# Performance work log

Measured on AMD Instinct MI355X. Metric: run time of the kernel, lower is better.

## Reference

```python
import jax, jax.numpy as jnp
import numpy as np

N = 100_000
E = 1_600_000
F_IN = 128
HID = 128
OUT = 64


def setup_inputs() -> dict:
    key = jax.random.key(0)
    k = jax.random.split(key, 6)
    x = jax.random.normal(k[0], (N, F_IN), dtype=jnp.float32)
    edge_index = jax.random.randint(k[1], (2, E), 0, N, dtype=jnp.int64)
    edge_weight = jax.random.uniform(k[2], (E,), dtype=jnp.float32)
    W1 = jax.random.normal(k[3], (F_IN, HID), dtype=jnp.float32) * (1.0 / np.sqrt(F_IN))
    b1 = jnp.zeros((HID,), dtype=jnp.float32)
    W2 = jax.random.normal(k[4], (HID, OUT), dtype=jnp.float32) * (1.0 / np.sqrt(HID))
    b2 = jnp.zeros((OUT,), dtype=jnp.float32)
    return {"x": x, "edge_index": edge_index, "edge_weight": edge_weight,
            "W1": W1, "b1": b1, "W2": W2, "b2": b2}


def reference(x, edge_index, edge_weight, W1, b1, W2, b2):
    n = x.shape[0]
    src, dst = edge_index[0], edge_index[1]
    # gcn_norm: add self-loops with weight 1
    loop = jnp.arange(n, dtype=src.dtype)
    src_f = jnp.concatenate([src, loop])          # [E+N]
    dst_f = jnp.concatenate([dst, loop])          # [E+N]
    w_f = jnp.concatenate([edge_weight, jnp.ones((n,), dtype=edge_weight.dtype)])
    # degree over target nodes, symmetric normalization D^-1/2 A D^-1/2
    deg = jax.ops.segment_sum(w_f, dst_f, num_segments=n)   # [N]
    dinv = jnp.where(deg > 0, jax.lax.rsqrt(deg), 0.0)
    norm = dinv[src_f] * w_f * dinv[dst_f]        # [E+N]
    # GCNConv: linear transform then normalized sparse aggregation + bias
    h = x @ W1                                    # [N, HID]
    msg = h[src_f] * norm[:, None]                # [E+N, HID] gather
    agg = jax.ops.segment_sum(msg, dst_f, num_segments=n) + b1  # scatter-add
    # ReLU + Linear
    return jax.nn.relu(agg) @ W2 + b2             # [N, OUT]
```

## Files before the change

### kernel.cpp

```cpp
#include <hip/hip_runtime.h>

#define N_NODES 100000
#define N_EDGES 1600000
#define F_IN    128
#define HID     128
#define F_OUT   64

#define NBUCK   196
#define NCHB    256
#define CHUNK_E (N_EDGES / NCHB)
#define GHN     (NBUCK * NCHB)

#define XB_BLKS (N_NODES * 16 / 256)
#define WC_BLKS ((HID * F_IN + F_OUT * HID + 255) / 256)

typedef __attribute__((ext_vector_type(8))) short bf16x8;
typedef __attribute__((ext_vector_type(4))) float f32x4;


__device__ __forceinline__ unsigned int bf16rn(float f) {
    unsigned int u = __float_as_uint(f);
    return (u + 0x7fffu + ((u >> 16) & 1u)) >> 16;
}
__device__ __forceinline__ float bf16tof(unsigned short h) {
    return __uint_as_float(((unsigned int)h) << 16);
}


__global__ __launch_bounds__(256) void k_pre(
        const float* __restrict__ x, unsigned short* __restrict__ xh,
        const float* __restrict__ W1, const float* __restrict__ W2,
        unsigned short* __restrict__ w1t, unsigned short* __restrict__ w2t,
        const int* __restrict__ dst, int* __restrict__ ghist) {
    __shared__ int bins[NBUCK];
    const int blk = blockIdx.x;
    const int t = threadIdx.x;
    if (blk < XB_BLKS) {
        int i = blk * 256 + t;
        float4 a = ((const float4*)x)[2 * i];
        float4 b = ((const float4*)x)[2 * i + 1];
        uint4 r;
        r.x = bf16rn(a.x) | (bf16rn(a.y) << 16);
        r.y = bf16rn(a.z) | (bf16rn(a.w) << 16);
        r.z = bf16rn(b.x) | (bf16rn(b.y) << 16);
        r.w = bf16rn(b.z) | (bf16rn(b.w) << 16);
        ((uint4*)xh)[i] = r;
    } else if (blk < XB_BLKS + WC_BLKS) {
        int i = (blk - XB_BLKS) * 256 + t;
        if (i < HID * F_IN) {
            int n = i >> 7, k = i & 127;
            w1t[i] = (unsigned short)bf16rn(W1[k * HID + n]);
        }
        int j = i - HID * F_IN;
        if (j >= 0 && j < F_OUT * HID) {
            int n = j >> 7, k = j & 127;
            w2t[j] = (unsigned short)bf16rn(W2[k * F_OUT + n]);
        }
    } else {
        int cb = blk - XB_BLKS - WC_BLKS;
        for (int j = t; j < NBUCK; j += 256) bins[j] = 0;
        __syncthreads();
        const int base = cb * CHUNK_E;
        for (int i = t; i < CHUNK_E; i += 256)
            atomicAdd(&bins[dst[base + i] >> 9], 1);
        __syncthreads();
        for (int j = t; j < NBUCK; j += 256)
            ghist[j * NCHB + cb] = bins[j];
    }
}


__global__ void k_scan_part(const int* __restrict__ data, int* __restrict__ part, int n) {
    int i = blockIdx.x * 256 + threadIdx.x;
    int v = (i < n) ? data[i] : 0;
    #pragma unroll
    for (int off = 32; off > 0; off >>= 1) v += __shfl_down(v, off, 64);
    __shared__ int ws[4];
    if ((threadIdx.x & 63) == 0) ws[threadIdx.x >> 6] = v;
    __syncthreads();
    if (threadIdx.x == 0) part[blockIdx.x] = ws[0] + ws[1] + ws[2] + ws[3];
}

__global__ __launch_bounds__(512) void k_scan_top(int* __restrict__ part, int nparts) {
    __shared__ int s[512];
    int t = threadIdx.x;
    int v = (t < nparts) ? part[t] : 0;
    s[t] = v;
    __syncthreads();
    for (int off = 1; off < 512; off <<= 1) {
        int u = (t >= off) ? s[t - off] : 0;
        __syncthreads();
        s[t] += u;
        __syncthreads();
    }
    if (t < nparts) part[t] = s[t] - v;
}

__global__ void k_scan_down(int* __restrict__ data, const int* __restrict__ part, int n) {
    __shared__ int s[256];
    int t = threadIdx.x;
    int i = blockIdx.x * 256 + t;
    int v = (i < n) ? data[i] : 0;
    s[t] = v;
    __syncthreads();
    for (int off = 1; off < 256; off <<= 1) {
        int u = (t >= off) ? s[t - off] : 0;
        __syncthreads();
        s[t] += u;
        __syncthreads();
    }
    if (i < n) data[i] = part[blockIdx.x] + s[t] - v;
}


__global__ __launch_bounds__(256) void k_bscatter(const int* __restrict__ src,
                                                  const int* __restrict__ dst,
                                                  const float* __restrict__ w,
                                                  const int* __restrict__ ghist,
                                                  int2* __restrict__ spw) {
    __shared__ int cur[NBUCK];
    const int t = threadIdx.x;
    const int blk = blockIdx.x;
    for (int j = t; j < NBUCK; j += 256) cur[j] = ghist[j * NCHB + blk];
    __syncthreads();
    const int base = blk * CHUNK_E;
    for (int i = t; i < CHUNK_E; i += 256) {
        int e = base + i;
        int d = dst[e];
        int b = d >> 9;
        int pos = atomicAdd(&cur[b], 1);
        int2 p;
        p.x = src[e] | ((d & 511) << 17);
        p.y = __float_as_int(w[e]);
        spw[pos] = p;
    }
}


__global__ __launch_bounds__(512) void k_csr(const int2* __restrict__ spw,
                                             const int* __restrict__ ghist,
                                             int* __restrict__ row_ptr,
                                             float* __restrict__ dinv,
                                             int2* __restrict__ pairs) {
    __shared__ int   scnt[512];
    __shared__ float swsum[512];
    __shared__ int   sexcl[512];
    const int t = threadIdx.x;
    const int b = blockIdx.x;
    const int bstart = ghist[b * NCHB];
    const int bend   = (b == NBUCK - 1) ? N_EDGES : ghist[(b + 1) * NCHB];
    const int ne = bend - bstart;

    scnt[t] = 0; swsum[t] = 0.0f;
    __syncthreads();
    for (int i = t; i < ne; i += 512) {
        int2 pe = spw[bstart + i];
        int dl = pe.x >> 17;
        atomicAdd(&scnt[dl], 1);
        atomicAdd(&swsum[dl], __int_as_float(pe.y));
    }
    __syncthreads();

    sexcl[t] = scnt[t];
    __syncthreads();
    for (int off = 1; off < 512; off <<= 1) {
        int u = (t >= off) ? sexcl[t - off] : 0;
        __syncthreads();
        sexcl[t] += u;
        __syncthreads();
    }
    int excl = sexcl[t] - scnt[t];

    int node = b * 512 + t;
    if (node < N_NODES) {
        row_ptr[node] = bstart + excl;
        dinv[node] = rsqrtf(1.0f + swsum[t]);
    }
    if (b == NBUCK - 1 && t == 0) row_ptr[N_NODES] = N_EDGES;

    sexcl[t] = excl;
    __syncthreads();
    scnt[t] = 0;
    __syncthreads();

    for (int i = t; i < ne; i += 512) {
        int2 pe = spw[bstart + i];
        int dl = pe.x >> 17;
        int r = atomicAdd(&scnt[dl], 1);
        int2 q;
        q.x = pe.x & 0x1FFFF;
        q.y = pe.y;
        pairs[bstart + sexcl[dl] + r] = q;
    }
}


__global__ __launch_bounds__(512) void k_gmlp(
        const int2* __restrict__ pairs,
        const int* __restrict__ row_ptr,
        const float* __restrict__ dinv,
        const unsigned short* __restrict__ xh,
        const unsigned short* __restrict__ w1t,
        const float* __restrict__ b1,
        const unsigned short* __restrict__ w2t,
        const float* __restrict__ b2,
        float* __restrict__ out) {
    __shared__ unsigned short gt[16][128];
    __shared__ unsigned short ht[16][128];

    const int t = threadIdx.x;
    const int row0 = blockIdx.x * 16;

    {
        const int grp  = t >> 5;
        const int lane = t & 31;
        const int n = row0 + grp;
        const float dn = dinv[n];
        const ushort4* xh4 = (const ushort4*)xh;

        ushort4 sv = xh4[n * 32 + lane];
        float4 acc;
        acc.x = dn * bf16tof(sv.x);
        acc.y = dn * bf16tof(sv.y);
        acc.z = dn * bf16tof(sv.z);
        acc.w = dn * bf16tof(sv.w);

        int beg = row_ptr[n];
        int end = row_ptr[n + 1];
        int e = beg;
        for (; e + 3 < end; e += 4) {
            int2 p0 = pairs[e];
            int2 p1 = pairs[e + 1];
            int2 p2 = pairs[e + 2];
            int2 p3 = pairs[e + 3];
            float nw0 = dinv[p0.x] * __int_as_float(p0.y);
            float nw1 = dinv[p1.x] * __int_as_float(p1.y);
            float nw2 = dinv[p2.x] * __int_as_float(p2.y);
            float nw3 = dinv[p3.x] * __int_as_float(p3.y);
            ushort4 v0 = xh4[p0.x * 32 + lane];
            ushort4 v1 = xh4[p1.x * 32 + lane];
            ushort4 v2 = xh4[p2.x * 32 + lane];
            ushort4 v3 = xh4[p3.x * 32 + lane];
            acc.x += nw0 * bf16tof(v0.x); acc.y += nw0 * bf16tof(v0.y);
            acc.z += nw0 * bf16tof(v0.z); acc.w += nw0 * bf16tof(v0.w);
            acc.x += nw1 * bf16tof(v1.x); acc.y += nw1 * bf16tof(v1.y);
            acc.z += nw1 * bf16tof(v1.z); acc.w += nw1 * bf16tof(v1.w);
            acc.x += nw2 * bf16tof(v2.x); acc.y += nw2 * bf16tof(v2.y);
            acc.z += nw2 * bf16tof(v2.z); acc.w += nw2 * bf16tof(v2.w);
            acc.x += nw3 * bf16tof(v3.x); acc.y += nw3 * bf16tof(v3.y);
            acc.z += nw3 * bf16tof(v3.z); acc.w += nw3 * bf16tof(v3.w);
        }
        for (; e < end; ++e) {
            int2 p = pairs[e];
            float nw = dinv[p.x] * __int_as_float(p.y);
            ushort4 v = xh4[p.x * 32 + lane];
            acc.x += nw * bf16tof(v.x); acc.y += nw * bf16tof(v.y);
            acc.z += nw * bf16tof(v.z); acc.w += nw * bf16tof(v.w);
        }
        acc.x *= dn; acc.y *= dn; acc.z *= dn; acc.w *= dn;

        uint2 r;
        r.x = bf16rn(acc.x) | (bf16rn(acc.y) << 16);
        r.y = bf16rn(acc.z) | (bf16rn(acc.w) << 16);
        *(uint2*)&gt[grp][(lane * 4) ^ ((grp & 7) << 3)] = r;
    }
    __syncthreads();

    const int wv   = t >> 6;
    const int lane = t & 63;
    const int r16  = lane & 15;
    const int g    = lane >> 4;
    const int swr  = (r16 & 7) << 3;

    {
        bf16x8 a[4];
        #pragma unroll
        for (int kt = 0; kt < 4; ++kt)
            a[kt] = *(const bf16x8*)&gt[r16][(kt * 32 + g * 8) ^ swr];

        f32x4 acc = {0.f, 0.f, 0.f, 0.f};
        const unsigned short* bcol = w1t + (wv * 16 + r16) * HID + g * 8;
        #pragma unroll
        for (int kt = 0; kt < 4; ++kt) {
            bf16x8 b = *(const bf16x8*)(bcol + kt * 32);
            acc = __builtin_amdgcn_mfma_f32_16x16x32_bf16(a[kt], b, acc, 0, 0, 0);
        }
        float bias = b1[wv * 16 + r16];
        #pragma unroll
        for (int q = 0; q < 4; ++q) {
            int row = g * 4 + q;
            float v = fmaxf(acc[q] + bias, 0.0f);
            ht[row][(wv * 16 + r16) ^ ((row & 7) << 3)] = (unsigned short)bf16rn(v);
        }
    }
    __syncthreads();

    if (wv < 4) {
        bf16x8 a2[4];
        #pragma unroll
        for (int kt = 0; kt < 4; ++kt)
            a2[kt] = *(const bf16x8*)&ht[r16][(kt * 32 + g * 8) ^ swr];

        f32x4 acc = {0.f, 0.f, 0.f, 0.f};
        const unsigned short* bcol = w2t + (wv * 16 + r16) * HID + g * 8;
        #pragma unroll
        for (int kt = 0; kt < 4; ++kt) {
            bf16x8 b = *(const bf16x8*)(bcol + kt * 32);
            acc = __builtin_amdgcn_mfma_f32_16x16x32_bf16(a2[kt], b, acc, 0, 0, 0);
        }
        float bias = b2[wv * 16 + r16];
        #pragma unroll
        for (int q = 0; q < 4; ++q)
            out[(size_t)(row0 + g * 4 + q) * F_OUT + wv * 16 + r16] = acc[q] + bias;
    }
}


extern "C" void kernel_launch(void* const* d_in, const int* in_sizes, int n_in,
                              void* d_out, int out_size, void* d_ws, size_t ws_size,
                              hipStream_t stream) {
    const float* x  = (const float*)d_in[0];
    const int*   ei = (const int*)d_in[1];
    const float* ew = (const float*)d_in[2];
    const float* W1 = (const float*)d_in[3];
    const float* b1 = (const float*)d_in[4];
    const float* W2 = (const float*)d_in[5];
    const float* b2 = (const float*)d_in[6];
    float* out = (float*)d_out;

    const int* src = ei;
    const int* dst = ei + N_EDGES;

    char* base = (char*)d_ws;
    auto alloc16 = [&](size_t bytes) { char* p = base; base += (bytes + 15) & ~(size_t)15; return p; };

    float*          dinv    = (float*)         alloc16(N_NODES * 4);
    unsigned short* xh      = (unsigned short*)alloc16((size_t)N_NODES * F_IN * 2);
    int*            row_ptr = (int*)           alloc16((N_NODES + 1) * 4);
    int*            ghist   = (int*)           alloc16(GHN * 4);
    int*            part    = (int*)           alloc16(256 * 4);
    int2*           pairs   = (int2*)          alloc16((size_t)N_EDGES * 8);
    int2*           spw     = (int2*)          alloc16((size_t)N_EDGES * 8);
    unsigned short* w1t     = (unsigned short*)alloc16(HID * F_IN * 2);
    unsigned short* w2t     = (unsigned short*)alloc16(F_OUT * HID * 2);

    const int GH_BLKS = (GHN + 255) / 256;

    k_pre<<<XB_BLKS + WC_BLKS + NCHB, 256, 0, stream>>>(x, xh, W1, W2, w1t, w2t, dst, ghist);
    k_scan_part<<<GH_BLKS, 256, 0, stream>>>(ghist, part, GHN);
    k_scan_top<<<1, 512, 0, stream>>>(part, GH_BLKS);
    k_scan_down<<<GH_BLKS, 256, 0, stream>>>(ghist, part, GHN);
    k_bscatter<<<NCHB, 256, 0, stream>>>(src, dst, ew, ghist, spw);
    k_csr<<<NBUCK, 512, 0, stream>>>(spw, ghist, row_ptr, dinv, pairs);
    k_gmlp<<<N_NODES / 16, 512, 0, stream>>>(pairs, row_ptr, dinv, xh, w1t, b1, w2t, b2, out);
}
```

Measured before the change: 176.2 us.

## Balance edge aggregation across groups via block-level edge splitting with LDS atomics

Instead of each 32-thread group aggregating all in-edges of one node, the block's full edge range is split evenly across the 16 groups. Each group walks its slice, accumulates per destination-row segment, and adds partial sums into a shared fp32 tile with LDS atomics. This evens out load imbalance from varying node degrees inside a block. In exchange it adds a row search, extra synchronisation, LDS atomic traffic, and more shared memory per block.

```diff
diff --git a/kernel.cpp b/kernel.cpp
--- a/kernel.cpp
+++ b/kernel.cpp
@@ -205,71 +205,95 @@
         const unsigned short* __restrict__ w2t,
         const float* __restrict__ b2,
         float* __restrict__ out) {
+    __shared__ float at[16][128];
     __shared__ unsigned short gt[16][128];
     __shared__ unsigned short ht[16][128];
+    __shared__ int rp[17];
 
     const int t = threadIdx.x;
     const int row0 = blockIdx.x * 16;
+    const int grp  = t >> 5;
+    const int lane = t & 31;
+    const ushort4* xh4 = (const ushort4*)xh;
+
+    if (t < 17) rp[t] = row_ptr[row0 + t];
+
+    const int n = row0 + grp;
+    const float dn = dinv[n];
+    ushort4 sv = xh4[n * 32 + lane];
+    at[grp][lane * 4 + 0] = dn * bf16tof(sv.x);
+    at[grp][lane * 4 + 1] = dn * bf16tof(sv.y);
+    at[grp][lane * 4 + 2] = dn * bf16tof(sv.z);
+    at[grp][lane * 4 + 3] = dn * bf16tof(sv.w);
+    __syncthreads();
 
     {
-        const int grp  = t >> 5;
-        const int lane = t & 31;
-        const int n = row0 + grp;
-        const float dn = dinv[n];
-        const ushort4* xh4 = (const ushort4*)xh;
-
-        ushort4 sv = xh4[n * 32 + lane];
-        float4 acc;
-        acc.x = dn * bf16tof(sv.x);
-        acc.y = dn * bf16tof(sv.y);
-        acc.z = dn * bf16tof(sv.z);
-        acc.w = dn * bf16tof(sv.w);
-
-        int beg = row_ptr[n];
-        int end = row_ptr[n + 1];
-        int e = beg;
-        for (; e + 3 < end; e += 4) {
-            int2 p0 = pairs[e];
-            int2 p1 = pairs[e + 1];
-            int2 p2 = pairs[e + 2];
-            int2 p3 = pairs[e + 3];
-            float nw0 = dinv[p0.x] * __int_as_float(p0.y);
-            float nw1 = dinv[p1.x] * __int_as_float(p1.y);
-            float nw2 = dinv[p2.x] * __int_as_float(p2.y);
-            float nw3 = dinv[p3.x] * __int_as_float(p3.y);
-            ushort4 v0 = xh4[p0.x * 32 + lane];
-            ushort4 v1 = xh4[p1.x * 32 + lane];
-            ushort4 v2 = xh4[p2.x * 32 + lane];
-            ushort4 v3 = xh4[p3.x * 32 + lane];
-            acc.x += nw0 * bf16tof(v0.x); acc.y += nw0 * bf16tof(v0.y);
-            acc.z += nw0 * bf16tof(v0.z); acc.w += nw0 * bf16tof(v0.w);
-            acc.x += nw1 * bf16tof(v1.x); acc.y += nw1 * bf16tof(v1.y);
-            acc.z += nw1 * bf16tof(v1.z); acc.w += nw1 * bf16tof(v1.w);
-            acc.x += nw2 * bf16tof(v2.x); acc.y += nw2 * bf16tof(v2.y);
-            acc.z += nw2 * bf16tof(v2.z); acc.w += nw2 * bf16tof(v2.w);
-            acc.x += nw3 * bf16tof(v3.x); acc.y += nw3 * bf16tof(v3.y);
-            acc.z += nw3 * bf16tof(v3.z); acc.w += nw3 * bf16tof(v3.w);
-        }
-        for (; e < end; ++e) {
-            int2 p = pairs[e];
-            float nw = dinv[p.x] * __int_as_float(p.y);
-            ushort4 v = xh4[p.x * 32 + lane];
-            acc.x += nw * bf16tof(v.x); acc.y += nw * bf16tof(v.y);
-            acc.z += nw * bf16tof(v.z); acc.w += nw * bf16tof(v.w);
-        }
-        acc.x *= dn; acc.y *= dn; acc.z *= dn; acc.w *= dn;
-
+        const int ebeg = rp[0], eend = rp[16];
+        const int cpg = (eend - ebeg + 15) >> 4;
+        int e  = ebeg + grp * cpg;
+        int e1 = e + cpg;
+        if (e1 > eend) e1 = eend;
+        if (e < e1) {
+            int row = 0;
+            while (rp[row + 1] <= e) ++row;
+            while (e < e1) {
+                while (rp[row + 1] <= e) ++row;
+                int send = rp[row + 1] < e1 ? rp[row + 1] : e1;
+                float4 acc = {0.f, 0.f, 0.f, 0.f};
+                for (; e + 3 < send; e += 4) {
+                    int2 p0 = pairs[e];
+                    int2 p1 = pairs[e + 1];
+                    int2 p2 = pairs[e + 2];
+                    int2 p3 = pairs[e + 3];
+                    float nw0 = dinv[p0.x] * __int_as_float(p0.y);
+                    float nw1 = dinv[p1.x] * __int_as_float(p1.y);
+                    float nw2 = dinv[p2.x] * __int_as_float(p2.y);
+                    float nw3 = dinv[p3.x] * __int_as_float(p3.y);
+                    ushort4 v0 = xh4[p0.x * 32 + lane];
+                    ushort4 v1 = xh4[p1.x * 32 + lane];
+                    ushort4 v2 = xh4[p2.x * 32 + lane];
+                    ushort4 v3 = xh4[p3.x * 32 + lane];
+                    acc.x += nw0 * bf16tof(v0.x); acc.y += nw0 * bf16tof(v0.y);
+                    acc.z += nw0 * bf16tof(v0.z); acc.w += nw0 * bf16tof(v0.w);
+                    acc.x += nw1 * bf16tof(v1.x); acc.y += nw1 * bf16tof(v1.y);
+                    acc.z += nw1 * bf16tof(v1.z); acc.w += nw1 * bf16tof(v1.w);
+                    acc.x += nw2 * bf16tof(v2.x); acc.y += nw2 * bf16tof(v2.y);
+                    acc.z += nw2 * bf16tof(v2.z); acc.w += nw2 * bf16tof(v2.w);
+                    acc.x += nw3 * bf16tof(v3.x); acc.y += nw3 * bf16tof(v3.y);
+                    acc.z += nw3 * bf16tof(v3.z); acc.w += nw3 * bf16tof(v3.w);
+                }
+                for (; e < send; ++e) {
+                    int2 p = pairs[e];
+                    float nw = dinv[p.x] * __int_as_float(p.y);
+                    ushort4 v = xh4[p.x * 32 + lane];
+                    acc.x += nw * bf16tof(v.x); acc.y += nw * bf16tof(v.y);
+                    acc.z += nw * bf16tof(v.z); acc.w += nw * bf16tof(v.w);
+                }
+                atomicAdd(&at[row][lane * 4 + 0], acc.x);
+                atomicAdd(&at[row][lane * 4 + 1], acc.y);
+                atomicAdd(&at[row][lane * 4 + 2], acc.z);
+                atomicAdd(&at[row][lane * 4 + 3], acc.w);
+            }
+        }
+    }
+    __syncthreads();
+
+    {
+        float ax0 = at[grp][lane * 4 + 0] * dn;
+        float ax1 = at[grp][lane * 4 + 1] * dn;
+        float ax2 = at[grp][lane * 4 + 2] * dn;
+        float ax3 = at[grp][lane * 4 + 3] * dn;
         uint2 r;
-        r.x = bf16rn(acc.x) | (bf16rn(acc.y) << 16);
-        r.y = bf16rn(acc.z) | (bf16rn(acc.w) << 16);
+        r.x = bf16rn(ax0) | (bf16rn(ax1) << 16);
+        r.y = bf16rn(ax2) | (bf16rn(ax3) << 16);
         *(uint2*)&gt[grp][(lane * 4) ^ ((grp & 7) << 3)] = r;
     }
     __syncthreads();
 
     const int wv   = t >> 6;
-    const int lane = t & 63;
-    const int r16  = lane & 15;
-    const int g    = lane >> 4;
+    const int wl   = t & 63;
+    const int r16  = wl & 15;
+    const int g    = wl >> 4;
     const int swr  = (r16 & 7) << 3;
 
     {
```

Measured after the change: 250.6 us. 1.42x slower.

## Split fused gather+MLP kernel into separate gather and MFMA MLP kernels

Applied to the files above, without the earlier changes.

Breaks the fused gather-then-MLP kernel into two kernels. The first is a standalone neighbor gather that writes the aggregated bf16 features to a workspace buffer, and that buffer reuses the spw scratch space. The second is an MLP kernel where each wave independently handles 16 rows across all output tiles. The aim is to decouple the latency-bound gather from the MFMA phase so neither stalls the other at block-wide barriers, and to let each run at its own occupancy. The cost is an extra round trip of the 100000x128 bf16 intermediate through global memory and one more kernel launch.

```diff
diff --git a/kernel.cpp b/kernel.cpp
--- a/kernel.cpp
+++ b/kernel.cpp
@@ -195,123 +195,130 @@
 }
 
 
-__global__ __launch_bounds__(512) void k_gmlp(
-        const int2* __restrict__ pairs,
-        const int* __restrict__ row_ptr,
-        const float* __restrict__ dinv,
-        const unsigned short* __restrict__ xh,
+__global__ __launch_bounds__(256) void k_gather(const int2* __restrict__ pairs,
+                                                const int* __restrict__ row_ptr,
+                                                const float* __restrict__ dinv,
+                                                const unsigned short* __restrict__ xh,
+                                                unsigned short* __restrict__ axh) {
+    int t = blockIdx.x * 256 + threadIdx.x;
+    int n = t >> 5;
+    int lane = t & 31;
+    if (n >= N_NODES) return;
+
+    const ushort4* xh4 = (const ushort4*)xh;
+    float dn = dinv[n];
+    ushort4 sv = xh4[n * 32 + lane];
+    float4 acc;
+    acc.x = dn * bf16tof(sv.x);
+    acc.y = dn * bf16tof(sv.y);
+    acc.z = dn * bf16tof(sv.z);
+    acc.w = dn * bf16tof(sv.w);
+
+    int beg = row_ptr[n];
+    int end = row_ptr[n + 1];
+    int e = beg;
+    for (; e + 3 < end; e += 4) {
+        int2 p0 = pairs[e];
+        int2 p1 = pairs[e + 1];
+        int2 p2 = pairs[e + 2];
+        int2 p3 = pairs[e + 3];
+        float nw0 = dinv[p0.x] * __int_as_float(p0.y);
+        float nw1 = dinv[p1.x] * __int_as_float(p1.y);
+        float nw2 = dinv[p2.x] * __int_as_float(p2.y);
+        float nw3 = dinv[p3.x] * __int_as_float(p3.y);
+        ushort4 v0 = xh4[p0.x * 32 + lane];
+        ushort4 v1 = xh4[p1.x * 32 + lane];
+        ushort4 v2 = xh4[p2.x * 32 + lane];
+        ushort4 v3 = xh4[p3.x * 32 + lane];
+        acc.x += nw0 * bf16tof(v0.x); acc.y += nw0 * bf16tof(v0.y);
+        acc.z += nw0 * bf16tof(v0.z); acc.w += nw0 * bf16tof(v0.w);
+        acc.x += nw1 * bf16tof(v1.x); acc.y += nw1 * bf16tof(v1.y);
+        acc.z += nw1 * bf16tof(v1.z); acc.w += nw1 * bf16tof(v1.w);
+        acc.x += nw2 * bf16tof(v2.x); acc.y += nw2 * bf16tof(v2.y);
+        acc.z += nw2 * bf16tof(v2.z); acc.w += nw2 * bf16tof(v2.w);
+        acc.x += nw3 * bf16tof(v3.x); acc.y += nw3 * bf16tof(v3.y);
+        acc.z += nw3 * bf16tof(v3.z); acc.w += nw3 * bf16tof(v3.w);
+    }
+    for (; e < end; ++e) {
+        int2 p = pairs[e];
+        float nw = dinv[p.x] * __int_as_float(p.y);
+        ushort4 v = xh4[p.x * 32 + lane];
+        acc.x += nw * bf16tof(v.x); acc.y += nw * bf16tof(v.y);
+        acc.z += nw * bf16tof(v.z); acc.w += nw * bf16tof(v.w);
+    }
+    acc.x *= dn; acc.y *= dn; acc.z *= dn; acc.w *= dn;
+    uint2 r;
+    r.x = bf16rn(acc.x) | (bf16rn(acc.y) << 16);
+    r.y = bf16rn(acc.z) | (bf16rn(acc.w) << 16);
+    ((uint2*)axh)[n * 32 + lane] = r;
+}
+
+
+__global__ __launch_bounds__(256) void k_mlp(
+        const unsigned short* __restrict__ axh,
         const unsigned short* __restrict__ w1t,
         const float* __restrict__ b1,
         const unsigned short* __restrict__ w2t,
         const float* __restrict__ b2,
         float* __restrict__ out) {
-    __shared__ unsigned short gt[16][128];
-    __shared__ unsigned short ht[16][128];
-
-    const int t = threadIdx.x;
-    const int row0 = blockIdx.x * 16;
-
-    {
-        const int grp  = t >> 5;
-        const int lane = t & 31;
-        const int n = row0 + grp;
-        const float dn = dinv[n];
-        const ushort4* xh4 = (const ushort4*)xh;
-
-        ushort4 sv = xh4[n * 32 + lane];
-        float4 acc;
-        acc.x = dn * bf16tof(sv.x);
-        acc.y = dn * bf16tof(sv.y);
-        acc.z = dn * bf16tof(sv.z);
-        acc.w = dn * bf16tof(sv.w);
-
-        int beg = row_ptr[n];
-        int end = row_ptr[n + 1];
-        int e = beg;
-        for (; e + 3 < end; e += 4) {
-            int2 p0 = pairs[e];
-            int2 p1 = pairs[e + 1];
-            int2 p2 = pairs[e + 2];
-            int2 p3 = pairs[e + 3];
-            float nw0 = dinv[p0.x] * __int_as_float(p0.y);
-            float nw1 = dinv[p1.x] * __int_as_float(p1.y);
-            float nw2 = dinv[p2.x] * __int_as_float(p2.y);
-            float nw3 = dinv[p3.x] * __int_as_float(p3.y);
-            ushort4 v0 = xh4[p0.x * 32 + lane];
-            ushort4 v1 = xh4[p1.x * 32 + lane];
-            ushort4 v2 = xh4[p2.x * 32 + lane];
-            ushort4 v3 = xh4[p3.x * 32 + lane];
-            acc.x += nw0 * bf16tof(v0.x); acc.y += nw0 * bf16tof(v0.y);
-            acc.z += nw0 * bf16tof(v0.z); acc.w += nw0 * bf16tof(v0.w);
-            acc.x += nw1 * bf16tof(v1.x); acc.y += nw1 * bf16tof(v1.y);
-            acc.z += nw1 * bf16tof(v1.z); acc.w += nw1 * bf16tof(v1.w);
-            acc.x += nw2 * bf16tof(v2.x); acc.y += nw2 * bf16tof(v2.y);
-            acc.z += nw2 * bf16tof(v2.z); acc.w += nw2 * bf16tof(v2.w);
-            acc.x += nw3 * bf16tof(v3.x); acc.y += nw3 * bf16tof(v3.y);
-            acc.z += nw3 * bf16tof(v3.z); acc.w += nw3 * bf16tof(v3.w);
-        }
-        for (; e < end; ++e) {
-            int2 p = pairs[e];
-            float nw = dinv[p.x] * __int_as_float(p.y);
-            ushort4 v = xh4[p.x * 32 + lane];
-            acc.x += nw * bf16tof(v.x); acc.y += nw * bf16tof(v.y);
-            acc.z += nw * bf16tof(v.z); acc.w += nw * bf16tof(v.w);
-        }
-        acc.x *= dn; acc.y *= dn; acc.z *= dn; acc.w *= dn;
-
-        uint2 r;
-        r.x = bf16rn(acc.x) | (bf16rn(acc.y) << 16);
-        r.y = bf16rn(acc.z) | (bf16rn(acc.w) << 16);
-        *(uint2*)&gt[grp][(lane * 4) ^ ((grp & 7) << 3)] = r;
-    }
-    __syncthreads();
-
-    const int wv   = t >> 6;
-    const int lane = t & 63;
-    const int r16  = lane & 15;
-    const int g    = lane >> 4;
-    const int swr  = (r16 & 7) << 3;
-
-    {
-        bf16x8 a[4];
-        #pragma unroll
-        for (int kt = 0; kt < 4; ++kt)
-            a[kt] = *(const bf16x8*)&gt[r16][(kt * 32 + g * 8) ^ swr];
-
+    __shared__ unsigned short hbuf[4][16][128];
+
+    const int wid  = threadIdx.x >> 6;
+    const int lane = threadIdx.x & 63;
+    const int r = lane & 15;
+    const int g = lane >> 4;
+
+    const int row0 = (blockIdx.x * 4 + wid) * 16;
+    const bool valid = (row0 + 16 <= N_NODES);
+    const int row0s = valid ? row0 : 0;
+
+    bf16x8 a[4];
+    const unsigned short* arow = axh + (size_t)(row0s + r) * HID + g * 8;
+    #pragma unroll
+    for (int kt = 0; kt < 4; ++kt)
+        a[kt] = *(const bf16x8*)(arow + kt * 32);
+
+    const int swr = (r & 7) << 3;
+
+    #pragma unroll
+    for (int nt = 0; nt < 8; ++nt) {
         f32x4 acc = {0.f, 0.f, 0.f, 0.f};
-        const unsigned short* bcol = w1t + (wv * 16 + r16) * HID + g * 8;
+        const unsigned short* bcol = w1t + (nt * 16 + r) * HID + g * 8;
         #pragma unroll
         for (int kt = 0; kt < 4; ++kt) {
             bf16x8 b = *(const bf16x8*)(bcol + kt * 32);
             acc = __builtin_amdgcn_mfma_f32_16x16x32_bf16(a[kt], b, acc, 0, 0, 0);
         }
-        float bias = b1[wv * 16 + r16];
+        float bias = b1[nt * 16 + r];
         #pragma unroll
         for (int q = 0; q < 4; ++q) {
             int row = g * 4 + q;
             float v = fmaxf(acc[q] + bias, 0.0f);
-            ht[row][(wv * 16 + r16) ^ ((row & 7) << 3)] = (unsigned short)bf16rn(v);
-        }
-    }
-    __syncthreads();
-
-    if (wv < 4) {
-        bf16x8 a2[4];
-        #pragma unroll
-        for (int kt = 0; kt < 4; ++kt)
-            a2[kt] = *(const bf16x8*)&ht[r16][(kt * 32 + g * 8) ^ swr];
-
+            hbuf[wid][row][(nt * 16 + r) ^ ((row & 7) << 3)] = (unsigned short)bf16rn(v);
+        }
+    }
+    __syncthreads();
+
+    bf16x8 a2[4];
+    #pragma unroll
+    for (int kt = 0; kt < 4; ++kt)
+        a2[kt] = *(const bf16x8*)(&hbuf[wid][r][(kt * 32 + g * 8) ^ swr]);
+
+    #pragma unroll
+    for (int nt = 0; nt < 4; ++nt) {
         f32x4 acc = {0.f, 0.f, 0.f, 0.f};
-        const unsigned short* bcol = w2t + (wv * 16 + r16) * HID + g * 8;
+        const unsigned short* bcol = w2t + (nt * 16 + r) * HID + g * 8;
         #pragma unroll
         for (int kt = 0; kt < 4; ++kt) {
             bf16x8 b = *(const bf16x8*)(bcol + kt * 32);
             acc = __builtin_amdgcn_mfma_f32_16x16x32_bf16(a2[kt], b, acc, 0, 0, 0);
         }
-        float bias = b2[wv * 16 + r16];
-        #pragma unroll
-        for (int q = 0; q < 4; ++q)
-            out[(size_t)(row0 + g * 4 + q) * F_OUT + wv * 16 + r16] = acc[q] + bias;
+        if (valid) {
+            float bias = b2[nt * 16 + r];
+            #pragma unroll
+            for (int q = 0; q < 4; ++q)
+                out[(size_t)(row0 + g * 4 + q) * F_OUT + nt * 16 + r] = acc[q] + bias;
+        }
     }
 }
 
@@ -340,9 +347,12 @@
     int*            ghist   = (int*)           alloc16(GHN * 4);
     int*            part    = (int*)           alloc16(256 * 4);
     int2*           pairs   = (int2*)          alloc16((size_t)N_EDGES * 8);
-    int2*           spw     = (int2*)          alloc16((size_t)N_EDGES * 8);
+    char*           big     =                  alloc16((size_t)N_NODES * HID * 2);
     unsigned short* w1t     = (unsigned short*)alloc16(HID * F_IN * 2);
     unsigned short* w2t     = (unsigned short*)alloc16(F_OUT * HID * 2);
+
+    int2*           spw     = (int2*)big;
+    unsigned short* axh     = (unsigned short*)big;
 
     const int GH_BLKS = (GHN + 255) / 256;
 
@@ -352,5 +362,6 @@
     k_scan_down<<<GH_BLKS, 256, 0, stream>>>(ghist, part, GHN);
     k_bscatter<<<NCHB, 256, 0, stream>>>(src, dst, ew, ghist, spw);
     k_csr<<<NBUCK, 512, 0, stream>>>(spw, ghist, row_ptr, dinv, pairs);
-    k_gmlp<<<N_NODES / 16, 512, 0, stream>>>(pairs, row_ptr, dinv, xh, w1t, b1, w2t, b2, out);
-}
+    k_gather<<<(N_NODES * 32 + 255) / 256, 256, 0, stream>>>(pairs, row_ptr, dinv, xh, axh);
+    k_mlp<<<(N_NODES / 16 + 3) / 4, 256, 0, stream>>>(axh, w1t, b1, w2t, b2, out);
+}
```

After: 187.4 us. +6.3%, slower.
